# Kernel optimization log

Hardware: AMD Instinct MI355X
Metric: run time of the kernel (lower is better)

## Reference

```python
import jax, jax.numpy as jnp
import numpy as np
import math

D_MODEL = 2048
N_HEADS = 16
D_K = D_MODEL // N_HEADS


def setup_inputs() -> dict:
    key = jax.random.key(0)
    k0, k1, k2, k3, k4 = jax.random.split(key, 5)
    B, T = 2, 2048
    x = jax.random.normal(k0, (B, T, D_MODEL), dtype=jnp.float32)
    s = 1.0 / math.sqrt(D_MODEL)
    W_qkv = jax.random.normal(k1, (3 * D_MODEL, D_MODEL), dtype=jnp.float32) * s
    b_qkv = jax.random.normal(k2, (3 * D_MODEL,), dtype=jnp.float32) * 0.01
    W_out = jax.random.normal(k3, (D_MODEL, D_MODEL), dtype=jnp.float32) * s
    b_out = jax.random.normal(k4, (D_MODEL,), dtype=jnp.float32) * 0.01
    return {"x": x, "W_qkv": W_qkv, "b_qkv": b_qkv, "W_out": W_out, "b_out": b_out}


def reference(x, W_qkv, b_qkv, W_out, b_out):
    B, T, C = x.shape
    qkv = x @ W_qkv.T + b_qkv                      # [B,T,3C]
    q, k, v = jnp.split(qkv, 3, axis=-1)
    # [B,T,C] -> [B,H,T,Dk]
    def to_heads(t):
        return t.reshape(B, T, N_HEADS, D_K).transpose(0, 2, 1, 3)
    q, k, v = to_heads(q), to_heads(k), to_heads(v)
    scale = 1.0 / math.sqrt(D_K)
    scores = jnp.einsum('bhqd,bhkd->bhqk', q, k) * scale   # [B,H,T,T]
    causal = jnp.tril(jnp.ones((T, T), dtype=bool))
    neg = jnp.finfo(scores.dtype).min
    scores = jnp.where(causal[None, None], scores, neg)
    attn = jax.nn.softmax(scores, axis=-1)
    out = jnp.einsum('bhqk,bhkd->bhqd', attn, v)           # [B,H,T,Dk]
    out = out.transpose(0, 2, 1, 3).reshape(B, T, C)
    return out @ W_out.T + b_out
```

## Files before the change

kernel.cpp:

```cpp
#include <hip/hip_runtime.h>
#include <stdint.h>

typedef short bf16x8 __attribute__((ext_vector_type(8)));
typedef float f32x4 __attribute__((ext_vector_type(4)));
typedef float f32x16 __attribute__((ext_vector_type(16)));
typedef unsigned short u16;
typedef unsigned int u32;

__device__ __forceinline__ u16 f2bf(float f) {
    u32 x = __float_as_uint(f);
    x += 0x7fffu + ((x >> 16) & 1u);
    return (u16)(x >> 16);
}
__device__ __forceinline__ u32 pack_bf2(float a, float b) {
    return (u32)f2bf(a) | ((u32)f2bf(b) << 16);
}

union Frag4 { u32 u[4]; bf16x8 v; };

__device__ __forceinline__ void gload16(const u16* g, u16* l) {
    __builtin_amdgcn_global_load_lds(
        (__attribute__((address_space(1))) void*)g,
        (__attribute__((address_space(3))) void*)l,
        16, 0, 0);
}

__global__ void cvt_f32_bf16(const float* __restrict__ in, u16* __restrict__ out, long n8) {
    long stride = (long)gridDim.x * blockDim.x;
    for (long i = (long)blockIdx.x * blockDim.x + threadIdx.x; i < n8; i += stride) {
        const float4* p = (const float4*)(in + i * 8);
        float4 a = p[0], b = p[1];
        uint4 o;
        o.x = pack_bf2(a.x, a.y);
        o.y = pack_bf2(a.z, a.w);
        o.z = pack_bf2(b.x, b.y);
        o.w = pack_bf2(b.z, b.w);
        ((uint4*)out)[i] = o;
    }
}

template<int OBF>
__global__ __launch_bounds__(256) void gemm_nt(
    const u16* __restrict__ A, const u16* __restrict__ B,
    const float* __restrict__ bias, void* __restrict__ out,
    int K, int ldo, int gxsh)
{
    __shared__ __align__(16) u16 lA[128 * 64];
    __shared__ __align__(16) u16 lB[128 * 64];
    const int tid  = threadIdx.x;
    const int lane = tid & 63;
    const int w    = tid >> 6;
    const int wm = (w >> 1) * 64, wn = (w & 1) * 64;

    const int nwg = gridDim.x;
    const int bid = blockIdx.x;
    const int swz = (bid & 7) * (nwg >> 3) + (bid >> 3);
    const int bm = (swz & ((1 << gxsh) - 1)) * 128;
    const int bn = (swz >> gxsh) * 128;

    const int lr = lane >> 3;
    const u32 sb = (u32)((lane & 7) * 16);

    f32x4 acc[4][4];
#pragma unroll
    for (int i = 0; i < 4; ++i)
#pragma unroll
        for (int j = 0; j < 4; ++j)
#pragma unroll
            for (int r = 0; r < 4; ++r) acc[i][j][r] = 0.f;

    for (int k0 = 0; k0 < K; k0 += 64) {
#pragma unroll
        for (int i = 0; i < 4; ++i) {
            const int c = w * 4 + i;
            const int row = c * 8 + lr;
            const u32 col = (sb ^ ((u32)(row & 7) << 4)) >> 1;
            gload16(A + (size_t)(bm + row) * K + k0 + col, lA + c * 512);
            gload16(B + (size_t)(bn + row) * K + k0 + col, lB + c * 512);
        }
        __syncthreads();
#pragma unroll
        for (int kk = 0; kk < 2; ++kk) {
            bf16x8 af[4], bfr[4];
#pragma unroll
            for (int f = 0; f < 4; ++f) {
                const int m = wm + f * 16 + (lane & 15);
                const u32 byt = (u32)(kk * 64 + (lane >> 4) * 16) ^ ((u32)(m & 7) << 4);
                af[f]  = *(const bf16x8*)((const char*)lA + m * 128 + byt);
                const int n = wn + f * 16 + (lane & 15);
                const u32 bytb = (u32)(kk * 64 + (lane >> 4) * 16) ^ ((u32)(n & 7) << 4);
                bfr[f] = *(const bf16x8*)((const char*)lB + n * 128 + bytb);
            }
#pragma unroll
            for (int i = 0; i < 4; ++i)
#pragma unroll
                for (int j = 0; j < 4; ++j)
                    acc[i][j] = __builtin_amdgcn_mfma_f32_16x16x32_bf16(af[i], bfr[j], acc[i][j], 0, 0, 0);
        }
        __syncthreads();
    }
#pragma unroll
    for (int i = 0; i < 4; ++i) {
        int m0 = bm + wm + i * 16 + ((lane >> 4) << 2);
#pragma unroll
        for (int j = 0; j < 4; ++j) {
            int n = bn + wn + j * 16 + (lane & 15);
            float bv = bias[n];
#pragma unroll
            for (int r = 0; r < 4; ++r) {
                float v = acc[i][j][r] + bv;
                if constexpr (OBF != 0)
                    ((u16*)out)[(size_t)(m0 + r) * ldo + n] = f2bf(v);
                else
                    ((float*)out)[(size_t)(m0 + r) * ldo + n] = v;
            }
        }
    }
}

__global__ __launch_bounds__(256) void transpose_v(
    const u16* __restrict__ qkv, u16* __restrict__ vt)
{
    __shared__ u16 lt[64 * 64];
    const int tid = threadIdx.x;
    const int bid = blockIdx.x;
    const int tt    = bid & 31;
    const int dtile = (bid >> 5) & 1;
    const int h     = (bid >> 6) & 15;
    const int b     = bid >> 10;
    const u16* src = qkv + ((size_t)b * 2048 + tt * 64) * 6144 + 4096 + h * 128 + dtile * 64;

    const int r = tid >> 2, ce = (tid & 3) * 16;
    uint4 a0 = *(const uint4*)(src + (size_t)r * 6144 + ce);
    uint4 a1 = *(const uint4*)(src + (size_t)r * 6144 + ce + 8);
    const u32 swz = (u32)((r & 7) << 4);
    *(uint4*)((char*)lt + r * 128 + (((u32)(ce * 2)) ^ swz)) = a0;
    *(uint4*)((char*)lt + r * 128 + (((u32)(ce * 2 + 16)) ^ swz)) = a1;
    __syncthreads();

    const int d = tid >> 2;
    u16* dst = vt + ((size_t)(b * 16 + h) * 128 + dtile * 64 + d) * 2048 + tt * 64;
#pragma unroll
    for (int it = 0; it < 2; ++it) {
        const int t0 = (tid & 3) * 8 + it * 32;
        union { u16 hh[8]; uint4 q4; } u;
#pragma unroll
        for (int uu = 0; uu < 8; ++uu) {
            int trow = t0 + uu;
            u32 byt = (u32)(trow * 128) + (((u32)(d * 2)) ^ ((u32)((trow & 7) << 4)));
            u.hh[uu] = *(const u16*)((const char*)lt + byt);
        }
        *(uint4*)(dst + t0) = u.q4;
    }
}

__global__ __launch_bounds__(256) void attn_fwd(
    const u16* __restrict__ qkv, const u16* __restrict__ vt,
    u16* __restrict__ obuf)
{
    __shared__ __align__(16) u16 lK[2 * 64 * 128];
    __shared__ __align__(16) u16 lV[2 * 128 * 64];
    const int tid  = threadIdx.x;
    const int lane = tid & 63;
    const int w    = tid >> 6;
    const int g    = lane >> 5;
    const int ql   = lane & 31;

    const int bid = blockIdx.x;
    const int qi  = bid >> 5;
    const int bh  = bid & 31;
    const int qtile = (qi < 8) ? (15 - qi) : (qi - 8);
    const int b = bh >> 4, h = bh & 15;
    const size_t rowbase = (size_t)b * 2048;
    const int qb = qtile * 128;
    const int qw = qb + w * 32;
    const int q  = qw + ql;
    const int nt = 2 * qtile + 2;

    const u16* Khead = qkv + rowbase * 6144 + 2048 + h * 128;
    const u16* Vth   = vt + (size_t)bh * 128 * 2048;

    bf16x8 qf[8];
    {
        const u16* qrow = qkv + (rowbase + q) * 6144 + h * 128;
#pragma unroll
        for (int ch = 0; ch < 8; ++ch)
            qf[ch] = *(const bf16x8*)(qrow + ch * 16 + g * 8);
    }

    f32x16 acc[4];
#pragma unroll
    for (int dt = 0; dt < 4; ++dt)
#pragma unroll
        for (int r = 0; r < 16; ++r) acc[dt][r] = 0.f;

    float m_run = -1e30f, l_run = 0.f;
    const float C2 = 0.08838834764831845f * 1.44269504088896341f;

    auto stage = [&](int bb, int t) {
        const int kb = t * 64;
#pragma unroll
        for (int i = 0; i < 4; ++i) {
            const int c = w * 4 + i;
            const int kr = c * 4 + (lane >> 4);
            const u32 kcol = (((u32)((lane & 15) * 16)) ^ ((u32)(kr & 7) << 4)) >> 1;
            gload16(Khead + (size_t)(kb + kr) * 6144 + kcol,
                    lK + bb * 8192 + c * 512);
            const int vr = c * 8 + (lane >> 3);
            const u32 vcol = (((u32)((lane & 7) * 16)) ^ ((u32)(vr & 7) << 4)) >> 1;
            gload16(Vth + (size_t)vr * 2048 + kb + vcol,
                    lV + bb * 8192 + c * 512);
        }
    };

    stage(0, 0);
    __syncthreads();
    int buf = 0;

    for (int t = 0; t < nt; ++t) {
        const int kb = t * 64;
        if (t + 1 < nt) stage(buf ^ 1, t + 1);

        if (kb <= qw + 31) {
            const char* lKb = (const char*)(lK + buf * 8192);
            const char* lVb = (const char*)(lV + buf * 8192);
#pragma unroll
            for (int s = 0; s < 2; ++s) {
                const int kb2 = kb + s * 32;
                if (kb2 > qw + 31) break;
                const bool diag = (kb2 == qw);

                bf16x8 kf[8];
                const u32 krow = (u32)(s * 32 + ql);
                const u32 ksw = (krow & 7) << 4;
#pragma unroll
                for (int ch = 0; ch < 8; ++ch)
                    kf[ch] = *(const bf16x8*)(lKb + krow * 256 + (((u32)(ch * 32 + g * 16)) ^ ksw));

                f32x16 s_;
#pragma unroll
                for (int r = 0; r < 16; ++r) s_[r] = 0.f;
                __builtin_amdgcn_s_setprio(1);
#pragma unroll
                for (int ch = 0; ch < 8; ++ch)
                    s_ = __builtin_amdgcn_mfma_f32_32x32x16_bf16(kf[ch], qf[ch], s_, 0, 0, 0);
                __builtin_amdgcn_s_setprio(0);

                float p[16];
                float tmax = -1e30f;
#pragma unroll
                for (int r = 0; r < 16; ++r) {
                    int crow = (r & 3) + 8 * (r >> 2) + 4 * g;
                    float v = s_[r];
                    if (diag && (crow > ql)) v = -1e30f;
                    p[r] = v;
                    tmax = fmaxf(tmax, v);
                }
                tmax = fmaxf(tmax, __shfl_xor(tmax, 32));
                if (!__all(tmax <= m_run + 8.0f)) {
                    float mnew  = fmaxf(m_run, tmax);
                    float alpha = exp2f((m_run - mnew) * C2);
#pragma unroll
                    for (int dt = 0; dt < 4; ++dt) acc[dt] = acc[dt] * alpha;
                    l_run *= alpha;
                    m_run = mnew;
                }
                float ssum = 0.f;
#pragma unroll
                for (int r = 0; r < 16; ++r) {
                    float e = exp2f((p[r] - m_run) * C2);
                    p[r] = e;
                    ssum += e;
                }
                ssum += __shfl_xor(ssum, 32);
                l_run += ssum;

                u32 wb[8], sw[8];
#pragma unroll
                for (int j = 0; j < 8; ++j) wb[j] = pack_bf2(p[2 * j], p[2 * j + 1]);
#pragma unroll
                for (int j = 0; j < 8; ++j) sw[j] = __shfl_xor(wb[j], 32);
                Frag4 pf0, pf1;
#pragma unroll
                for (int u = 0; u < 4; ++u) {
                    const bool own = (g == (u >> 1));
                    pf0.u[u] = own ? wb[2 * g + (u & 1)]     : sw[2 * g + (u & 1)];
                    pf1.u[u] = own ? wb[4 + 2 * g + (u & 1)] : sw[4 + 2 * g + (u & 1)];
                }

                __builtin_amdgcn_s_setprio(1);
#pragma unroll
                for (int dt = 0; dt < 4; ++dt) {
                    const u32 vrow = (u32)(dt * 32 + ql);
                    const u32 vsw = (vrow & 7) << 4;
                    bf16x8 v0 = *(const bf16x8*)(lVb + vrow * 128 + (((u32)(s * 64 + g * 16)) ^ vsw));
                    bf16x8 v1 = *(const bf16x8*)(lVb + vrow * 128 + (((u32)(s * 64 + 32 + g * 16)) ^ vsw));
                    acc[dt] = __builtin_amdgcn_mfma_f32_32x32x16_bf16(v0, pf0.v, acc[dt], 0, 0, 0);
                    acc[dt] = __builtin_amdgcn_mfma_f32_32x32x16_bf16(v1, pf1.v, acc[dt], 0, 0, 0);
                }
                __builtin_amdgcn_s_setprio(0);
            }
        }
        __syncthreads();
        buf ^= 1;
    }

    const float inv_l = 1.0f / l_run;
    u16* orow = obuf + (rowbase + q) * 2048 + h * 128;
#pragma unroll
    for (int dt = 0; dt < 4; ++dt) {
#pragma unroll
        for (int rr = 0; rr < 4; ++rr) {
            int d0 = dt * 32 + rr * 8 + g * 4;
            int r0 = rr * 4;
            u32 w0 = pack_bf2(acc[dt][r0] * inv_l,     acc[dt][r0 + 1] * inv_l);
            u32 w1 = pack_bf2(acc[dt][r0 + 2] * inv_l, acc[dt][r0 + 3] * inv_l);
            *(u32*)(orow + d0)     = w0;
            *(u32*)(orow + d0 + 2) = w1;
        }
    }
}

extern "C" void kernel_launch(void* const* d_in, const int* in_sizes, int n_in,
                              void* d_out, int out_size, void* d_ws, size_t ws_size,
                              hipStream_t stream) {
    (void)in_sizes; (void)n_in; (void)out_size; (void)ws_size;
    const float* x    = (const float*)d_in[0];
    const float* Wqkv = (const float*)d_in[1];
    const float* bqkv = (const float*)d_in[2];
    const float* Wout = (const float*)d_in[3];
    const float* bout = (const float*)d_in[4];

    char* ws = (char*)d_ws;
    u16* xb  = (u16*)ws;
    u16* wqb = (u16*)(ws + (size_t)16777216);
    u16* qkv = (u16*)(ws + (size_t)41943040);
    u16* ob  = xb;
    u16* vtb = wqb;
    u16* wob = wqb;

    cvt_f32_bf16<<<2048, 256, 0, stream>>>(x, xb, 8388608L / 8);
    cvt_f32_bf16<<<2048, 256, 0, stream>>>(Wqkv, wqb, 12582912L / 8);
    gemm_nt<1><<<1536, 256, 0, stream>>>(xb, wqb, bqkv, qkv, 2048, 6144, 5);
    transpose_v<<<2048, 256, 0, stream>>>(qkv, vtb);
    attn_fwd<<<512, 256, 0, stream>>>(qkv, vtb, ob);
    cvt_f32_bf16<<<2048, 256, 0, stream>>>(Wout, wob, 4194304L / 8);
    gemm_nt<0><<<512, 256, 0, stream>>>(ob, wob, bout, d_out, 2048, 2048, 5);
}
```

Measured before the change: 365.6 us.

## Process full 64-key tile per online-softmax step in attention loop

Merges the two 32-key sub-steps of each 64-key tile into a single softmax update: both QK^T score blocks are computed together, one max and rescale check covers 64 keys, and the PV MFMAs run back to back. The row-sum cross-lane shuffle is moved out of the loop to a single reduction at the end. This cuts per-tile rescale, shuffle and branch overhead and gives more independent MFMA work, at the cost of higher register pressure from doubled K fragments and P arrays.

```diff
diff --git a/kernel.cpp b/kernel.cpp
--- a/kernel.cpp
+++ b/kernel.cpp
@@ -224,87 +224,126 @@
         if (kb <= qw + 31) {
             const char* lKb = (const char*)(lK + buf * 8192);
             const char* lVb = (const char*)(lV + buf * 8192);
-#pragma unroll
-            for (int s = 0; s < 2; ++s) {
-                const int kb2 = kb + s * 32;
-                if (kb2 > qw + 31) break;
-                const bool diag = (kb2 == qw);
-
-                bf16x8 kf[8];
-                const u32 krow = (u32)(s * 32 + ql);
-                const u32 ksw = (krow & 7) << 4;
+            const bool f1 = (kb >= qw);
+            const bool m0 = (kb == qw);
+            const bool m1 = (kb + 32 == qw);
+
+            bf16x8 kf0[8], kf1[8];
+            const u32 kr0 = (u32)ql, kr1 = (u32)(32 + ql);
+            const u32 ks0 = (kr0 & 7) << 4, ks1 = (kr1 & 7) << 4;
+#pragma unroll
+            for (int ch = 0; ch < 8; ++ch) {
+                const u32 byt = (u32)(ch * 32 + g * 16);
+                kf0[ch] = *(const bf16x8*)(lKb + kr0 * 256 + (byt ^ ks0));
+                kf1[ch] = *(const bf16x8*)(lKb + kr1 * 256 + (byt ^ ks1));
+            }
+            f32x16 s0_, s1_;
+#pragma unroll
+            for (int r = 0; r < 16; ++r) { s0_[r] = 0.f; s1_[r] = 0.f; }
+            __builtin_amdgcn_s_setprio(1);
+#pragma unroll
+            for (int ch = 0; ch < 8; ++ch)
+                s0_ = __builtin_amdgcn_mfma_f32_32x32x16_bf16(kf0[ch], qf[ch], s0_, 0, 0, 0);
+            if (!f1) {
 #pragma unroll
                 for (int ch = 0; ch < 8; ++ch)
-                    kf[ch] = *(const bf16x8*)(lKb + krow * 256 + (((u32)(ch * 32 + g * 16)) ^ ksw));
-
-                f32x16 s_;
-#pragma unroll
-                for (int r = 0; r < 16; ++r) s_[r] = 0.f;
-                __builtin_amdgcn_s_setprio(1);
-#pragma unroll
-                for (int ch = 0; ch < 8; ++ch)
-                    s_ = __builtin_amdgcn_mfma_f32_32x32x16_bf16(kf[ch], qf[ch], s_, 0, 0, 0);
-                __builtin_amdgcn_s_setprio(0);
-
-                float p[16];
-                float tmax = -1e30f;
+                    s1_ = __builtin_amdgcn_mfma_f32_32x32x16_bf16(kf1[ch], qf[ch], s1_, 0, 0, 0);
+            }
+            __builtin_amdgcn_s_setprio(0);
+
+            float p[32];
+#pragma unroll
+            for (int r = 0; r < 16; ++r) p[r] = s0_[r];
+            if (m0) {
 #pragma unroll
                 for (int r = 0; r < 16; ++r) {
                     int crow = (r & 3) + 8 * (r >> 2) + 4 * g;
-                    float v = s_[r];
-                    if (diag && (crow > ql)) v = -1e30f;
-                    p[r] = v;
-                    tmax = fmaxf(tmax, v);
+                    if (crow > ql) p[r] = -1e30f;
                 }
-                tmax = fmaxf(tmax, __shfl_xor(tmax, 32));
-                if (!__all(tmax <= m_run + 8.0f)) {
-                    float mnew  = fmaxf(m_run, tmax);
-                    float alpha = exp2f((m_run - mnew) * C2);
-#pragma unroll
-                    for (int dt = 0; dt < 4; ++dt) acc[dt] = acc[dt] * alpha;
-                    l_run *= alpha;
-                    m_run = mnew;
+            }
+            if (f1) {
+#pragma unroll
+                for (int r = 0; r < 16; ++r) p[16 + r] = -1e30f;
+            } else {
+#pragma unroll
+                for (int r = 0; r < 16; ++r) p[16 + r] = s1_[r];
+                if (m1) {
+#pragma unroll
+                    for (int r = 0; r < 16; ++r) {
+                        int crow = (r & 3) + 8 * (r >> 2) + 4 * g;
+                        if (crow > ql) p[16 + r] = -1e30f;
+                    }
                 }
-                float ssum = 0.f;
-#pragma unroll
-                for (int r = 0; r < 16; ++r) {
-                    float e = exp2f((p[r] - m_run) * C2);
-                    p[r] = e;
-                    ssum += e;
+            }
+            float mt[16];
+#pragma unroll
+            for (int i = 0; i < 16; ++i) mt[i] = fmaxf(p[i], p[i + 16]);
+#pragma unroll
+            for (int i = 0; i < 8; ++i) mt[i] = fmaxf(mt[i], mt[i + 8]);
+#pragma unroll
+            for (int i = 0; i < 4; ++i) mt[i] = fmaxf(mt[i], mt[i + 4]);
+            float tmax = fmaxf(fmaxf(mt[0], mt[1]), fmaxf(mt[2], mt[3]));
+
+            if (!__all(tmax <= m_run + 8.0f)) {
+                float jmax  = fmaxf(tmax, __shfl_xor(tmax, 32));
+                float mnew  = fmaxf(m_run, jmax);
+                float alpha = exp2f((m_run - mnew) * C2);
+#pragma unroll
+                for (int dt = 0; dt < 4; ++dt) acc[dt] = acc[dt] * alpha;
+                l_run *= alpha;
+                m_run = mnew;
+            }
+#pragma unroll
+            for (int r = 0; r < 32; ++r)
+                p[r] = exp2f((p[r] - m_run) * C2);
+            float st[16];
+#pragma unroll
+            for (int i = 0; i < 16; ++i) st[i] = p[i] + p[i + 16];
+#pragma unroll
+            for (int i = 0; i < 8; ++i) st[i] += st[i + 8];
+#pragma unroll
+            for (int i = 0; i < 4; ++i) st[i] += st[i + 4];
+            l_run += (st[0] + st[1]) + (st[2] + st[3]);
+
+            u32 wv[16], sw[16];
+#pragma unroll
+            for (int j = 0; j < 16; ++j) wv[j] = pack_bf2(p[2 * j], p[2 * j + 1]);
+#pragma unroll
+            for (int j = 0; j < 16; ++j) sw[j] = __shfl_xor(wv[j], 32);
+            Frag4 pf0, pf1, pf2, pf3;
+#pragma unroll
+            for (int u = 0; u < 4; ++u) {
+                const bool own = (g == (u >> 1));
+                const int i0 = 2 * g + (u & 1);
+                pf0.u[u] = own ? wv[i0]      : sw[i0];
+                pf1.u[u] = own ? wv[4 + i0]  : sw[4 + i0];
+                pf2.u[u] = own ? wv[8 + i0]  : sw[8 + i0];
+                pf3.u[u] = own ? wv[12 + i0] : sw[12 + i0];
+            }
+
+            __builtin_amdgcn_s_setprio(1);
+#pragma unroll
+            for (int dt = 0; dt < 4; ++dt) {
+                const u32 vrow = (u32)(dt * 32 + ql);
+                const u32 vsw = (vrow & 7) << 4;
+                bf16x8 v00 = *(const bf16x8*)(lVb + vrow * 128 + (((u32)(g * 16)) ^ vsw));
+                bf16x8 v01 = *(const bf16x8*)(lVb + vrow * 128 + (((u32)(32 + g * 16)) ^ vsw));
+                acc[dt] = __builtin_amdgcn_mfma_f32_32x32x16_bf16(v00, pf0.v, acc[dt], 0, 0, 0);
+                acc[dt] = __builtin_amdgcn_mfma_f32_32x32x16_bf16(v01, pf1.v, acc[dt], 0, 0, 0);
+                if (!f1) {
+                    bf16x8 v10 = *(const bf16x8*)(lVb + vrow * 128 + (((u32)(64 + g * 16)) ^ vsw));
+                    bf16x8 v11 = *(const bf16x8*)(lVb + vrow * 128 + (((u32)(96 + g * 16)) ^ vsw));
+                    acc[dt] = __builtin_amdgcn_mfma_f32_32x32x16_bf16(v10, pf2.v, acc[dt], 0, 0, 0);
+                    acc[dt] = __builtin_amdgcn_mfma_f32_32x32x16_bf16(v11, pf3.v, acc[dt], 0, 0, 0);
                 }
-                ssum += __shfl_xor(ssum, 32);
-                l_run += ssum;
-
-                u32 wb[8], sw[8];
-#pragma unroll
-                for (int j = 0; j < 8; ++j) wb[j] = pack_bf2(p[2 * j], p[2 * j + 1]);
-#pragma unroll
-                for (int j = 0; j < 8; ++j) sw[j] = __shfl_xor(wb[j], 32);
-                Frag4 pf0, pf1;
-#pragma unroll
-                for (int u = 0; u < 4; ++u) {
-                    const bool own = (g == (u >> 1));
-                    pf0.u[u] = own ? wb[2 * g + (u & 1)]     : sw[2 * g + (u & 1)];
-                    pf1.u[u] = own ? wb[4 + 2 * g + (u & 1)] : sw[4 + 2 * g + (u & 1)];
-                }
-
-                __builtin_amdgcn_s_setprio(1);
-#pragma unroll
-                for (int dt = 0; dt < 4; ++dt) {
-                    const u32 vrow = (u32)(dt * 32 + ql);
-                    const u32 vsw = (vrow & 7) << 4;
-                    bf16x8 v0 = *(const bf16x8*)(lVb + vrow * 128 + (((u32)(s * 64 + g * 16)) ^ vsw));
-                    bf16x8 v1 = *(const bf16x8*)(lVb + vrow * 128 + (((u32)(s * 64 + 32 + g * 16)) ^ vsw));
-                    acc[dt] = __builtin_amdgcn_mfma_f32_32x32x16_bf16(v0, pf0.v, acc[dt], 0, 0, 0);
-                    acc[dt] = __builtin_amdgcn_mfma_f32_32x32x16_bf16(v1, pf1.v, acc[dt], 0, 0, 0);
-                }
-                __builtin_amdgcn_s_setprio(0);
-            }
+            }
+            __builtin_amdgcn_s_setprio(0);
         }
         __syncthreads();
         buf ^= 1;
     }
 
+    l_run += __shfl_xor(l_run, 32);
     const float inv_l = 1.0f / l_run;
     u16* orow = obuf + (rowbase + q) * 2048 + h * 128;
 #pragma unroll
```

After: 387.1 us. 1.06x slower.

## Double-buffer LDS tiles in GEMM to overlap global loads with MFMA

Applied to the files above, without the earlier changes.

Adds a second LDS buffer for the A and B tiles in the NT GEMM and prefetches the tile two steps ahead, using explicit vmcnt waits and raw barriers so global-to-LDS loads overlap MFMA compute. It also raises wave priority around the MFMA block and sets launch bounds to two blocks per CU. The cost targeted is the load latency exposed by the old load-sync-compute-sync loop. In exchange LDS use doubles to 64KB per block, which may limit occupancy, and the hand-written waitcnt logic is fragile.

```diff
diff --git a/kernel.cpp b/kernel.cpp
--- a/kernel.cpp
+++ b/kernel.cpp
@@ -40,13 +40,13 @@
 }
 
 template<int OBF>
-__global__ __launch_bounds__(256) void gemm_nt(
+__global__ __launch_bounds__(256, 2) void gemm_nt(
     const u16* __restrict__ A, const u16* __restrict__ B,
     const float* __restrict__ bias, void* __restrict__ out,
     int K, int ldo, int gxsh)
 {
-    __shared__ __align__(16) u16 lA[128 * 64];
-    __shared__ __align__(16) u16 lB[128 * 64];
+    __shared__ __align__(16) u16 lA[2 * 128 * 64];
+    __shared__ __align__(16) u16 lB[2 * 128 * 64];
     const int tid  = threadIdx.x;
     const int lane = tid & 63;
     const int w    = tid >> 6;
@@ -60,25 +60,38 @@
 
     const int lr = lane >> 3;
     const u32 sb = (u32)((lane & 7) * 16);
-
-    f32x4 acc[4][4];
-#pragma unroll
-    for (int i = 0; i < 4; ++i)
-#pragma unroll
-        for (int j = 0; j < 4; ++j)
-#pragma unroll
-            for (int r = 0; r < 4; ++r) acc[i][j][r] = 0.f;
-
-    for (int k0 = 0; k0 < K; k0 += 64) {
+    const int NT = K >> 6;
+
+    auto stage = [&](int bb, int k0) {
 #pragma unroll
         for (int i = 0; i < 4; ++i) {
             const int c = w * 4 + i;
             const int row = c * 8 + lr;
             const u32 col = (sb ^ ((u32)(row & 7) << 4)) >> 1;
-            gload16(A + (size_t)(bm + row) * K + k0 + col, lA + c * 512);
-            gload16(B + (size_t)(bn + row) * K + k0 + col, lB + c * 512);
-        }
-        __syncthreads();
+            gload16(A + (size_t)(bm + row) * K + k0 + col, lA + bb * 8192 + c * 512);
+            gload16(B + (size_t)(bn + row) * K + k0 + col, lB + bb * 8192 + c * 512);
+        }
+    };
+
+    f32x4 acc[4][4];
+#pragma unroll
+    for (int i = 0; i < 4; ++i)
+#pragma unroll
+        for (int j = 0; j < 4; ++j)
+#pragma unroll
+            for (int r = 0; r < 4; ++r) acc[i][j][r] = 0.f;
+
+    stage(0, 0);
+    stage(1, 64);
+    asm volatile("s_waitcnt vmcnt(8)" ::: "memory");
+    __builtin_amdgcn_sched_barrier(0);
+    __builtin_amdgcn_s_barrier();
+    __builtin_amdgcn_sched_barrier(0);
+
+    for (int t = 0; t < NT; ++t) {
+        const int cur = t & 1;
+        const char* pA = (const char*)(lA + cur * 8192);
+        const char* pB = (const char*)(lB + cur * 8192);
 #pragma unroll
         for (int kk = 0; kk < 2; ++kk) {
             bf16x8 af[4], bfr[4];
@@ -86,19 +99,33 @@
             for (int f = 0; f < 4; ++f) {
                 const int m = wm + f * 16 + (lane & 15);
                 const u32 byt = (u32)(kk * 64 + (lane >> 4) * 16) ^ ((u32)(m & 7) << 4);
-                af[f]  = *(const bf16x8*)((const char*)lA + m * 128 + byt);
+                af[f]  = *(const bf16x8*)(pA + m * 128 + byt);
                 const int n = wn + f * 16 + (lane & 15);
                 const u32 bytb = (u32)(kk * 64 + (lane >> 4) * 16) ^ ((u32)(n & 7) << 4);
-                bfr[f] = *(const bf16x8*)((const char*)lB + n * 128 + bytb);
+                bfr[f] = *(const bf16x8*)(pB + n * 128 + bytb);
             }
+            __builtin_amdgcn_s_setprio(1);
 #pragma unroll
             for (int i = 0; i < 4; ++i)
 #pragma unroll
                 for (int j = 0; j < 4; ++j)
                     acc[i][j] = __builtin_amdgcn_mfma_f32_16x16x32_bf16(af[i], bfr[j], acc[i][j], 0, 0, 0);
-        }
-        __syncthreads();
-    }
+            __builtin_amdgcn_s_setprio(0);
+        }
+        __builtin_amdgcn_sched_barrier(0);
+        __builtin_amdgcn_s_barrier();
+        __builtin_amdgcn_sched_barrier(0);
+        if (t + 2 < NT) {
+            stage(cur, (t + 2) * 64);
+            asm volatile("s_waitcnt vmcnt(8)" ::: "memory");
+        } else {
+            asm volatile("s_waitcnt vmcnt(0)" ::: "memory");
+        }
+        __builtin_amdgcn_sched_barrier(0);
+        __builtin_amdgcn_s_barrier();
+        __builtin_amdgcn_sched_barrier(0);
+    }
+
 #pragma unroll
     for (int i = 0; i < 4; ++i) {
         int m0 = bm + wm + i * 16 + ((lane >> 4) << 2);
```

Result: faster. 349.8 us (-4.3%).
